# Kernel optimization log

Measured on AMD Instinct MI355X. Metric: run time of the kernel, lower is better.

Reference implementation:

```python
import jax, jax.numpy as jnp
import numpy as np

D_MODEL = 1024
D_K = 1024
B, T = 4, 2048


def setup_inputs() -> dict:
    key = jax.random.key(0)
    kx, kq, kk, kv = jax.random.split(key, 4)
    s = 1.0 / np.sqrt(D_MODEL)
    return {
        "x": jax.random.normal(kx, (B, T, D_MODEL), dtype=jnp.float32),
        "W_q": jax.random.normal(kq, (D_MODEL, D_K), dtype=jnp.float32) * s,
        "W_k": jax.random.normal(kk, (D_MODEL, D_K), dtype=jnp.float32) * s,
        "W_v": jax.random.normal(kv, (D_MODEL, D_K), dtype=jnp.float32) * s,
    }


def reference(x, W_q, W_k, W_v):
    # x: (B, T, C); W_*: (C, d_k). Linear(no bias) == x @ W
    q = jnp.einsum('btc,ck->btk', x, W_q)
    k = jnp.einsum('btc,ck->btk', x, W_k)
    v = jnp.einsum('btc,ck->btk', x, W_v)
    d_k = W_q.shape[1]
    scores = jnp.einsum('bqk,bsk->bqs', q, k) / jnp.sqrt(jnp.asarray(d_k, x.dtype))
    T_ = x.shape[1]
    causal = jnp.tril(jnp.ones((T_, T_), dtype=bool))
    scores = jnp.where(causal, scores, jnp.asarray(-jnp.inf, scores.dtype))
    weights = jax.nn.softmax(scores, axis=-1)
    return jnp.einsum('bqs,bsk->bqk', weights, v)
```

## Files before the change

kernel.cpp:

```cpp
#include <hip/hip_runtime.h>
#include <hip/hip_bf16.h>
#include <stdint.h>
#include <math.h>

typedef __bf16 bf16x8 __attribute__((ext_vector_type(8)));
typedef float  f32x4  __attribute__((ext_vector_type(4)));
typedef unsigned int u32x4 __attribute__((ext_vector_type(4)));

__device__ __forceinline__ unsigned short f2bf(float x) {
    union { float f; unsigned u; } v; v.f = x;
    unsigned r = v.u + 0x7fffu + ((v.u >> 16) & 1u);
    return (unsigned short)(r >> 16);
}

__device__ __forceinline__ float bf2f(unsigned short b) {
    union { unsigned u; float f; } v; v.u = ((unsigned)b) << 16; return v.f;
}

__device__ __forceinline__ void async16(const void* g, void* l) {
    __builtin_amdgcn_global_load_lds(
        (const __attribute__((address_space(1))) void*)g,
        (__attribute__((address_space(3))) void*)l,
        16, 0, 0);
}

template <typename OutT, bool KLIMIT, bool VFOLD, int ZMODE, int TN, int EPI>
__global__ __launch_bounds__(256, (TN == 128) ? 3 : 2) void gemm_bt(
    const unsigned short* __restrict__ A,
    const unsigned short* __restrict__ Bt,
    OutT* __restrict__ C,
    unsigned short* __restrict__ VtOut,
    float* __restrict__ RS,
    int M, int N, int K, int lda, int ldb, int ldc,
    int ldvt, int nsplit,
    long long sA, long long sB, long long sC, long long sVt, float scale)
{
    constexpr int NJ   = TN / 32;
    constexpr int BUFE = (TN == 128) ? 8192 : 12288;

    int bn, bm, bz;
    if constexpr (ZMODE == 1) {
        const int o = blockIdx.x, x = o & 7, q = o >> 3;
        bz = x >> 1;
        const int tile = (x & 1) * 96 + q * 4 + blockIdx.z;
        bn = tile / 16; bm = tile % 16;
    } else if constexpr (ZMODE == 2) {
        const int o = blockIdx.x, x = o & 7, q = o >> 3;
        bz = x >> 1;
        const int t = (x & 1) * 68 + q * 4 + blockIdx.z;
        int r = (int)((sqrtf(8.f * (float)t + 1.f) - 1.f) * 0.5f);
        while ((r + 1) * (r + 2) / 2 <= t) r++;
        while (r * (r + 1) / 2 > t) r--;
        bm = r; bn = t - r * (r + 1) / 2;
    } else if constexpr (ZMODE == 3) {
        const int o = blockIdx.x, x = o & 7, q = o >> 3;
        bz = x >> 1;
        const int tile = (x & 1) * 64 + q * 4 + blockIdx.z;
        bn = tile >> 4; bm = 15 - (tile & 15);
    } else {
        bn = blockIdx.x; bm = blockIdx.y; bz = blockIdx.z;
    }

    A  += (long long)bz * sA;
    Bt += (long long)bz * sB;
    C  += (long long)bz * sC;

    const int m0 = bm * 128, n0 = bn * TN;
    const int Keff = KLIMIT ? min(K, (bm + 1) * 128) : K;
    const int nsteps = Keff >> 5;

    __shared__ __align__(16) unsigned short LDS[3 * BUFE];
    __shared__ float LDSI[128];

    const int tid  = threadIdx.x;
    const int w    = tid >> 6, l = tid & 63;
    const int wr   = w >> 1,  wc = w & 1;
    const int lrow = l & 15,  quad = l >> 4;

    if constexpr (EPI == 2) {
        if (tid < 128) {
            const float* rp = RS + (long long)bz * 65536 + (m0 + tid);
            float rs = 0.f;
            for (int b = 0; b < 2 * (bm + 1); ++b) rs += rp[b * 2048];
            LDSI[tid] = 1.0f / rs;
        }
    }

    f32x4 acc[4][NJ] = {};

    const int cOff = (((l & 3) ^ ((l >> 3) & 3))) * 8;
    const unsigned short* aG0 = A + (long long)(m0 + 32 * w + (l >> 2))      * lda + cOff;
    const unsigned short* aG1 = A + (long long)(m0 + 32 * w + (l >> 2) + 16) * lda + cOff;
    const unsigned short* bG0 = Bt + (long long)(n0 + (TN / 4) * w + (l >> 2))      * ldb + cOff;
    const unsigned short* bG1 = Bt + (long long)(n0 + (TN / 4) * w + (l >> 2) + 16) * ldb + cOff;
    const unsigned short* bG2 = Bt + (long long)(n0 + (TN / 4) * w + (l >> 2) + 32) * ldb + cOff;
    const unsigned short* bG3 = Bt + (long long)(n0 + (TN / 4) * w + (l >> 2) + 48) * ldb + cOff;
    unsigned short* aL = &LDS[w * 1024 + l * 8];
    unsigned short* bL = &LDS[4096 + w * (TN * 8) + l * 8];

    const int sl = (lrow >> 1) & 3;

    auto STG = [&](int s) {
        const int off = (s % 3) * BUFE;
        const int kk  = s * 32;
        async16(aG0 + kk, aL + off);
        async16(aG1 + kk, aL + off + 512);
        async16(bG0 + kk, bL + off);
        async16(bG1 + kk, bL + off + 512);
        if constexpr (TN == 256) {
            async16(bG2 + kk, bL + off + 1024);
            async16(bG3 + kk, bL + off + 1536);
        }
    };

    STG(0);
    if (nsteps > 1) STG(1);

    for (int t = 0; t < nsteps; ++t) {
        if (t + 1 < nsteps) {
            if constexpr (TN == 128) asm volatile("s_waitcnt vmcnt(4)" ::: "memory");
            else                     asm volatile("s_waitcnt vmcnt(6)" ::: "memory");
        } else {
            asm volatile("s_waitcnt vmcnt(0)" ::: "memory");
        }
        __builtin_amdgcn_s_barrier();
        asm volatile("" ::: "memory");

        if (t + 2 < nsteps) STG(t + 2);

        const unsigned short* As = &LDS[(t % 3) * BUFE];
        const unsigned short* Bs = As + 4096;
        bf16x8 af[4], bfr[NJ];
#pragma unroll
        for (int i = 0; i < 4; i++)
            af[i]  = *(const bf16x8*)&As[(wr * 64 + i * 16 + lrow) * 32 + (quad ^ sl) * 8];
#pragma unroll
        for (int j = 0; j < NJ; j++)
            bfr[j] = *(const bf16x8*)&Bs[(wc * (TN / 2) + j * 16 + lrow) * 32 + (quad ^ sl) * 8];
#pragma unroll
        for (int i = 0; i < 4; i++)
#pragma unroll
            for (int j = 0; j < NJ; j++)
                acc[i][j] = __builtin_amdgcn_mfma_f32_16x16x32_bf16(af[i], bfr[j], acc[i][j], 0, 0, 0);
    }

    if constexpr (VFOLD) {
        if (n0 >= nsplit) {
            unsigned short* Vp = VtOut + (long long)bz * sVt;
#pragma unroll
            for (int i = 0; i < 4; i++) {
                const int t = m0 + wr * 64 + i * 16 + quad * 4;
#pragma unroll
                for (int j = 0; j < NJ; j++) {
                    const int d = (n0 - nsplit) + wc * (TN / 2) + j * 16 + lrow;
                    union { unsigned short u[4]; uint2 p; } o;
#pragma unroll
                    for (int r = 0; r < 4; r++) o.u[r] = f2bf(acc[i][j][r] * scale);
                    *(uint2*)(Vp + (long long)d * ldvt + t) = o.p;
                }
            }
            return;
        }
    }

    __syncthreads();

    const int erow = l >> 2, ep = l & 3;

    if constexpr (EPI == 1) {
        char* eb = (char*)LDS + w * 2288;
        float* rsp = RS + (long long)bz * 65536 + (bn * 2 + wc) * 2048;
#pragma unroll
        for (int i = 0; i < 4; i++) {
            float ev[4][4];
#pragma unroll
            for (int j = 0; j < 4; j++)
#pragma unroll
                for (int r = 0; r < 4; r++) {
                    const int grow = m0 + wr * 64 + i * 16 + quad * 4 + r;
                    const int gcol = n0 + wc * 64 + j * 16 + lrow;
                    float e = __expf(acc[i][j][r] * scale);
                    e = (gcol <= grow) ? e : 0.f;
                    const unsigned short qb = f2bf(e);
                    ev[j][r] = bf2f(qb);
                    *(unsigned short*)(eb + (quad * 4 + r) * 144 + (j * 16 + lrow) * 2) = qb;
                }
#pragma unroll
            for (int r = 0; r < 4; r++) {
                float p = ev[0][r] + ev[1][r] + ev[2][r] + ev[3][r];
                p += __shfl_xor(p, 1); p += __shfl_xor(p, 2);
                p += __shfl_xor(p, 4); p += __shfl_xor(p, 8);
                if (lrow == 0)
                    rsp[m0 + wr * 64 + i * 16 + quad * 4 + r] = p;
            }
            const long long gm = m0 + wr * 64 + i * 16 + erow;
#pragma unroll
            for (int c = 0; c < 2; c++) {
                u32x4 d = *(u32x4*)(eb + erow * 144 + ep * 32 + c * 16);
                *(u32x4*)((unsigned short*)C + gm * ldc + (n0 + wc * 64 + ep * 16 + c * 8)) = d;
            }
        }
    } else if constexpr (sizeof(OutT) == 2 && TN == 128) {
        char* eb = (char*)LDS + w * 2288;
#pragma unroll
        for (int i = 0; i < 4; i++) {
#pragma unroll
            for (int j = 0; j < 4; j++)
#pragma unroll
                for (int r = 0; r < 4; r++)
                    *(unsigned short*)(eb + (quad * 4 + r) * 144 + (j * 16 + lrow) * 2) =
                        f2bf(acc[i][j][r] * scale);
            const long long gm = m0 + wr * 64 + i * 16 + erow;
#pragma unroll
            for (int c = 0; c < 2; c++) {
                u32x4 d = *(u32x4*)(eb + erow * 144 + ep * 32 + c * 16);
                *(u32x4*)((unsigned short*)C + gm * ldc + (n0 + wc * 64 + ep * 16 + c * 8)) = d;
            }
        }
    } else if constexpr (sizeof(OutT) == 2 && TN == 256) {
        char* eb = (char*)LDS + w * 4352;
#pragma unroll
        for (int i = 0; i < 4; i++) {
#pragma unroll
            for (int j = 0; j < 8; j++)
#pragma unroll
                for (int r = 0; r < 4; r++)
                    *(unsigned short*)(eb + (quad * 4 + r) * 272 + (j * 16 + lrow) * 2) =
                        f2bf(acc[i][j][r] * scale);
            const long long gm = m0 + wr * 64 + i * 16 + erow;
#pragma unroll
            for (int c = 0; c < 4; c++) {
                u32x4 d = *(u32x4*)(eb + erow * 272 + ep * 64 + c * 16);
                *(u32x4*)((unsigned short*)C + gm * ldc + (n0 + wc * 128 + ep * 32 + c * 8)) = d;
            }
        }
    } else {
        char* eb = (char*)LDS + w * 2304;
#pragma unroll
        for (int i = 0; i < 4; i++) {
            const long long gm = m0 + wr * 64 + i * 16 + erow;
            float inv = 1.0f;
            if constexpr (EPI == 2) inv = LDSI[wr * 64 + i * 16 + erow];
#pragma unroll
            for (int jc = 0; jc < NJ / 2; jc++) {
#pragma unroll
                for (int jj = 0; jj < 2; jj++)
#pragma unroll
                    for (int r = 0; r < 4; r++)
                        *(float*)(eb + (quad * 4 + r) * 144 + (jj * 16 + lrow) * 4) =
                            acc[i][2 * jc + jj][r] * scale;
#pragma unroll
                for (int c = 0; c < 2; c++) {
                    f32x4 d = *(f32x4*)(eb + erow * 144 + ep * 32 + c * 16);
                    if constexpr (EPI == 2) d *= inv;
                    *(f32x4*)((float*)C + gm * ldc + (n0 + wc * (TN / 2) + jc * 32 + ep * 8 + c * 4)) = d;
                }
            }
        }
    }
}

__global__ __launch_bounds__(256) void prep_fused(
    const float4* __restrict__ xin, unsigned short* __restrict__ xout, int n4, int nCast,
    const float* __restrict__ W0, const float* __restrict__ W1,
    const float* __restrict__ W2, unsigned short* __restrict__ wout, int n)
{
    const int tid = threadIdx.x;
    if ((int)blockIdx.x < nCast) {
        int i = blockIdx.x * 256 + tid;
        if (i >= n4) return;
        float4 v = xin[i];
        union { unsigned short u[4]; uint2 p; } o;
        o.u[0] = f2bf(v.x); o.u[1] = f2bf(v.y); o.u[2] = f2bf(v.z); o.u[3] = f2bf(v.w);
        *(uint2*)(xout + (long long)i * 4) = o.p;
        return;
    }
    const int bx = blockIdx.x - nCast;
    const int wz = bx >> 10, rem = bx & 1023;
    const int wy = rem >> 5, wx = rem & 31;
    const float* in = (wz == 0) ? W0 : (wz == 1) ? W1 : W2;
    unsigned short* out = wout + (long long)wz * n * n;
    __shared__ float tile[32][33];
    const int tx = tid & 31, ty = tid >> 5;
    const int c0 = wx * 32, r0 = wy * 32;
#pragma unroll
    for (int i = 0; i < 4; i++)
        tile[ty + i * 8][tx] = in[(long long)(r0 + ty + i * 8) * n + c0 + tx];
    __syncthreads();
#pragma unroll
    for (int i = 0; i < 4; i++)
        out[(long long)(c0 + ty + i * 8) * n + r0 + tx] = f2bf(tile[tx][ty + i * 8]);
}

extern "C" void kernel_launch(void* const* d_in, const int* in_sizes, int n_in,
                              void* d_out, int out_size, void* d_ws, size_t ws_size,
                              hipStream_t stream)
{
    const int B = 4, T = 2048, C = 1024, D = 1024;
    const float* x  = (const float*)d_in[0];
    const float* Wq = (const float*)d_in[1];
    const float* Wk = (const float*)d_in[2];
    const float* Wv = (const float*)d_in[3];
    float* out = (float*)d_out;
    char* ws = (char*)d_ws;

    const size_t MB = 1ull << 20;
    unsigned short* Xbf   = (unsigned short*)(ws + 0);
    float*          RSP   = (float*)(ws + 0);
    unsigned short* WqkvT = (unsigned short*)(ws + 16 * MB);
    unsigned short* QK    = (unsigned short*)(ws + 22 * MB);
    unsigned short* Vt    = (unsigned short*)(ws + 54 * MB);
    unsigned short* Sbf   = (unsigned short*)(ws + 70 * MB);

    const long long sX  = (long long)T * C;
    const long long sQK = (long long)T * 2 * D;
    const long long sVt = (long long)D * T;
    const long long sS  = (long long)T * T;
    const long long sO  = (long long)T * D;

    {
        int n4 = B * T * C / 4;
        int nCast = (n4 + 255) / 256;
        prep_fused<<<dim3(nCast + 3072), dim3(256), 0, stream>>>(
            (const float4*)x, Xbf, n4, nCast, Wq, Wk, Wv, WqkvT, 1024);
    }
    {
        dim3 g(192, 1, 4), b(256);
        gemm_bt<unsigned short, false, true, 1, 256, 0><<<g, b, 0, stream>>>(
            Xbf, WqkvT, QK, Vt, nullptr, 2048, 3072, 1024, 1024, 1024, 2048,
             T,  2048, sX, 0, sQK, sVt, 1.0f);
    }
    {
        dim3 g(136, 1, 4), b(256);
        gemm_bt<unsigned short, false, false, 2, 128, 1><<<g, b, 0, stream>>>(
            QK, QK + D, Sbf, nullptr, RSP, 2048, 2048, 1024, 2 * D, 2 * D, 2048,
            0, 0, sQK, sQK, sS, 0, 0.03125f);
    }
    {
        dim3 g(128, 1, 4), b(256);
        gemm_bt<float, true, false, 3, 128, 2><<<g, b, 0, stream>>>(
            Sbf, Vt, out, nullptr, RSP, 2048, 1024, 2048, 2048, 2048, 1024,
            0, 0, sS, sVt, sO, 0, 1.0f);
    }
    (void)in_sizes; (void)n_in; (void)out_size; (void)ws_size;
}
```

Baseline: 247.7 us.

## Compute softmax row sums inside PV GEMM from loaded P fragments

Removes the partial row-sum reduction and global writes from the QK^T exp epilogue. The PV GEMM now sums the bf16 P values from the A fragments it already loads each K step, then reduces them across lanes to form the reciprocal normalizer. This drops the RS workspace traffic and the serial pre-loop reduction at the cost of extra VALU adds in the main loop. The sum covers only columns within Keff, which matches the causal mask because the masked entries are zero.

```diff
diff --git a/kernel.cpp b/kernel.cpp
--- a/kernel.cpp
+++ b/kernel.cpp
@@ -30,7 +30,6 @@
     const unsigned short* __restrict__ Bt,
     OutT* __restrict__ C,
     unsigned short* __restrict__ VtOut,
-    float* __restrict__ RS,
     int M, int N, int K, int lda, int ldb, int ldc,
     int ldvt, int nsplit,
     long long sA, long long sB, long long sC, long long sVt, float scale)
@@ -77,16 +76,8 @@
     const int wr   = w >> 1,  wc = w & 1;
     const int lrow = l & 15,  quad = l >> 4;
 
-    if constexpr (EPI == 2) {
-        if (tid < 128) {
-            const float* rp = RS + (long long)bz * 65536 + (m0 + tid);
-            float rs = 0.f;
-            for (int b = 0; b < 2 * (bm + 1); ++b) rs += rp[b * 2048];
-            LDSI[tid] = 1.0f / rs;
-        }
-    }
-
     f32x4 acc[4][NJ] = {};
+    float rsum[4] = {0.f, 0.f, 0.f, 0.f};
 
     const int cOff = (((l & 3) ^ ((l >> 3) & 3))) * 8;
     const unsigned short* aG0 = A + (long long)(m0 + 32 * w + (l >> 2))      * lda + cOff;
@@ -137,6 +128,17 @@
 #pragma unroll
         for (int j = 0; j < NJ; j++)
             bfr[j] = *(const bf16x8*)&Bs[(wc * (TN / 2) + j * 16 + lrow) * 32 + (quad ^ sl) * 8];
+
+        if constexpr (EPI == 2) {
+#pragma unroll
+            for (int i = 0; i < 4; i++) {
+                float s0 = 0.f;
+#pragma unroll
+                for (int e = 0; e < 8; e++) s0 += (float)af[i][e];
+                rsum[i] += s0;
+            }
+        }
+
 #pragma unroll
         for (int i = 0; i < 4; i++)
 #pragma unroll
@@ -163,16 +165,24 @@
         }
     }
 
+    if constexpr (EPI == 2) {
+#pragma unroll
+        for (int i = 0; i < 4; i++) {
+            float r = rsum[i];
+            r += __shfl_xor(r, 16);
+            r += __shfl_xor(r, 32);
+            if (quad == 0) LDSI[wr * 64 + i * 16 + lrow] = 1.0f / r;
+        }
+    }
+
     __syncthreads();
 
     const int erow = l >> 2, ep = l & 3;
 
     if constexpr (EPI == 1) {
         char* eb = (char*)LDS + w * 2288;
-        float* rsp = RS + (long long)bz * 65536 + (bn * 2 + wc) * 2048;
-#pragma unroll
-        for (int i = 0; i < 4; i++) {
-            float ev[4][4];
+#pragma unroll
+        for (int i = 0; i < 4; i++) {
 #pragma unroll
             for (int j = 0; j < 4; j++)
 #pragma unroll
@@ -181,18 +191,8 @@
                     const int gcol = n0 + wc * 64 + j * 16 + lrow;
                     float e = __expf(acc[i][j][r] * scale);
                     e = (gcol <= grow) ? e : 0.f;
-                    const unsigned short qb = f2bf(e);
-                    ev[j][r] = bf2f(qb);
-                    *(unsigned short*)(eb + (quad * 4 + r) * 144 + (j * 16 + lrow) * 2) = qb;
+                    *(unsigned short*)(eb + (quad * 4 + r) * 144 + (j * 16 + lrow) * 2) = f2bf(e);
                 }
-#pragma unroll
-            for (int r = 0; r < 4; r++) {
-                float p = ev[0][r] + ev[1][r] + ev[2][r] + ev[3][r];
-                p += __shfl_xor(p, 1); p += __shfl_xor(p, 2);
-                p += __shfl_xor(p, 4); p += __shfl_xor(p, 8);
-                if (lrow == 0)
-                    rsp[m0 + wr * 64 + i * 16 + quad * 4 + r] = p;
-            }
             const long long gm = m0 + wr * 64 + i * 16 + erow;
 #pragma unroll
             for (int c = 0; c < 2; c++) {
@@ -306,7 +306,6 @@
 
     const size_t MB = 1ull << 20;
     unsigned short* Xbf   = (unsigned short*)(ws + 0);
-    float*          RSP   = (float*)(ws + 0);
     unsigned short* WqkvT = (unsigned short*)(ws + 16 * MB);
     unsigned short* QK    = (unsigned short*)(ws + 22 * MB);
     unsigned short* Vt    = (unsigned short*)(ws + 54 * MB);
@@ -327,19 +326,19 @@
     {
         dim3 g(192, 1, 4), b(256);
         gemm_bt<unsigned short, false, true, 1, 256, 0><<<g, b, 0, stream>>>(
-            Xbf, WqkvT, QK, Vt, nullptr, 2048, 3072, 1024, 1024, 1024, 2048,
+            Xbf, WqkvT, QK, Vt, 2048, 3072, 1024, 1024, 1024, 2048,
              T,  2048, sX, 0, sQK, sVt, 1.0f);
     }
     {
         dim3 g(136, 1, 4), b(256);
         gemm_bt<unsigned short, false, false, 2, 128, 1><<<g, b, 0, stream>>>(
-            QK, QK + D, Sbf, nullptr, RSP, 2048, 2048, 1024, 2 * D, 2 * D, 2048,
+            QK, QK + D, Sbf, nullptr, 2048, 2048, 1024, 2 * D, 2 * D, 2048,
             0, 0, sQK, sQK, sS, 0, 0.03125f);
     }
     {
         dim3 g(128, 1, 4), b(256);
         gemm_bt<float, true, false, 3, 128, 2><<<g, b, 0, stream>>>(
-            Sbf, Vt, out, nullptr, RSP, 2048, 1024, 2048, 2048, 2048, 1024,
+            Sbf, Vt, out, nullptr, 2048, 1024, 2048, 2048, 2048, 1024,
             0, 0, sS, sVt, sO, 0, 1.0f);
     }
     (void)in_sizes; (void)n_in; (void)out_size; (void)ws_size;
```

After: 236.1 us. -4.7%, faster.
